# Optimization experiments

Measured on AMD Instinct MI355X. Metric: run time of the kernel, lower is better.

Reference implementation:

```python
import jax, jax.numpy as jnp
import numpy as np

SLOPE = 0.01  # torch LeakyReLU default negative_slope

def _leaky(v):
    return jnp.where(v >= 0, v, SLOPE * v)

def _conv3d(x, w, b, stride):
    y = jax.lax.conv_general_dilated(
        x, w, window_strides=(stride, stride, stride), padding='VALID',
        dimension_numbers=('NCDHW', 'OIDHW', 'NCDHW'))
    return y + b[None, :, None, None, None]

def setup_inputs() -> dict:
    key = jax.random.key(0)
    ks = jax.random.split(key, 12)
    s = 0.05  # small init scale to keep exp(L1) numerically sane
    x = jax.random.normal(ks[0], (64, 1, 92, 92, 92), dtype=jnp.float32)
    w1 = jax.random.normal(ks[1], (16, 1, 6, 6, 6), dtype=jnp.float32) * s
    b1 = jnp.zeros((16,), jnp.float32)
    w2 = jax.random.normal(ks[2], (32, 16, 5, 5, 5), dtype=jnp.float32) * s
    b2 = jnp.zeros((32,), jnp.float32)
    w3 = jax.random.normal(ks[3], (48, 32, 5, 5, 5), dtype=jnp.float32) * s
    b3 = jnp.zeros((48,), jnp.float32)
    w4 = jax.random.normal(ks[4], (64, 48, 3, 3, 3), dtype=jnp.float32) * s
    b4 = jnp.zeros((64,), jnp.float32)
    T = jax.random.normal(ks[5], (512, 64 * 16), dtype=jnp.float32) * s
    Wm = jax.random.normal(ks[6], (512 + 64, 1), dtype=jnp.float32) * s
    bm = jnp.zeros((1,), jnp.float32)
    return {'x': x, 'w1': w1, 'b1': b1, 'w2': w2, 'b2': b2, 'w3': w3,
            'b3': b3, 'w4': w4, 'b4': b4, 'T': T, 'Wm': Wm, 'bm': bm}

def reference(x, w1, b1, w2, b2, w3, b3, w4, b4, T, Wm, bm):
    h = _leaky(_conv3d(x, w1, b1, 2))   # [N,16,44,44,44]
    h = _leaky(_conv3d(h, w2, b2, 3))   # [N,32,14,14,14]
    h = _leaky(_conv3d(h, w3, b3, 3))   # [N,48,4,4,4]
    h = _leaky(_conv3d(h, w4, b4, 1))   # [N,64,2,2,2]
    feature = h.reshape(h.shape[0], -1)  # [N,512]
    # minibatch discrimination: M [N,64,16]
    M = (feature @ T).reshape(-1, 64, 16)
    # pairwise L1 over last dim -> [N,N,64]; sum_j exp(.) -> [N,64]
    dist = jnp.sum(jnp.abs(M[:, None, :, :] - M[None, :, :, :]), axis=-1)
    out_T = jnp.sum(jnp.exp(dist), axis=1)
    z = jnp.concatenate([feature, out_T], axis=1) @ Wm + bm
    return jax.nn.sigmoid(z)
```

## Files before the change

### kernel.cpp

```cpp
#include <hip/hip_runtime.h>
#include <hip/hip_bf16.h>
#include <hip/hip_fp16.h>

typedef _Float16 v2h __attribute__((ext_vector_type(2)));
typedef _Float16 v8h __attribute__((ext_vector_type(8)));
typedef __fp16  v2hf __attribute__((ext_vector_type(2)));
typedef float v4f __attribute__((ext_vector_type(4)));

static inline __device__ float leaky(float v) { return v >= 0.f ? v : 0.01f * v; }

static inline __device__ v2h pkrtz(float a, float b) {
    v2hf r = __builtin_amdgcn_cvt_pkrtz(a, b);
    return __builtin_bit_cast(v2h, r);
}

#define W4S_OFF   0
#define H3_OFF    1655808
#define FEAT_OFF  1852416
#define M_OFF     1885184
#define OT_OFF    1950720
#define F16_BASE  1954816
#define WL1_OFF   0
#define BF2_OFF   4608
#define BF3_OFF   81408
#define H2C_OFF   273408
#define H1C_OFF   5893120

__global__ void prep_kernel(const float* __restrict__ w1, const float* __restrict__ w2,
                            const float* __restrict__ w3, const float* __restrict__ w4,
                            float* __restrict__ w4s, _Float16* __restrict__ Bw1,
                            _Float16* __restrict__ Bf2, _Float16* __restrict__ Bf3) {
    int i = blockIdx.x * 256 + threadIdx.x;
    if (i < 4608) {
        int ks = i >> 9, l = (i >> 3) & 63, j = i & 7;
        int oc = l & 15, kg = l >> 4;
        int g = ks * 4 + kg;
        int kz = g / 6, ky = g % 6;
        Bw1[i] = (j < 6) ? (_Float16)w1[oc * 216 + kz * 36 + ky * 6 + j]
                         : (_Float16)0.f;
    } else if (i < 4608 + 76800) {
        int j2 = i - 4608;
        int nt = j2 / 38400, r = j2 % 38400;
        int t = r / 512, l = (r % 512) >> 3, j = r & 7;
        int oc = nt * 16 + (l & 15);
        int k = (l >> 4) * 8 + j;
        int kz = t / 15, ky = (t % 15) / 3, kxp = t % 3;
        int kx = kxp * 2 + (k >= 16 ? 1 : 0);
        int ic = k & 15;
        Bf2[j2] = (kx < 5) ? (_Float16)w2[oc * 2000 + ic * 125 + kz * 25 + ky * 5 + kx]
                           : (_Float16)0.f;
    } else if (i < 4608 + 76800 + 192000) {
        int j3 = i - (4608 + 76800);
        int nt = j3 / 64000, r = j3 % 64000;
        int tap = r / 512, l = (r % 512) >> 3, j = r & 7;
        int oc = nt * 16 + (l & 15);
        int ic = (l >> 4) * 8 + j;
        Bf3[j3] = (_Float16)w3[oc * 4000 + ic * 125 + tap];
    } else {
        int j4 = i - (4608 + 76800 + 192000);
        if (j4 < 110592) {
            int kx = j4 & 3, r = (j4 >> 2) % 9, ic = (j4 >> 2) / 9 % 48, oc = j4 / 1728;
            w4s[j4] = (kx < 3) ? w4[oc * 1296 + ic * 27 + r * 3 + kx] : 0.f;
        }
    }
}

__global__ __launch_bounds__(512, 4) void conv1_kernel(
    const float* __restrict__ x, const _Float16* __restrict__ Bw1,
    const float* __restrict__ b1, _Float16* __restrict__ h1c, int n0, int NT) {
    __shared__ __align__(16) _Float16 buf[2][13824];
    int tid = threadIdx.x;
    int lane = tid & 63, wv = tid >> 6;
    int col = lane & 15, kg = lane >> 4;
    int zl = wv & 3, yh = wv >> 2;

    int t0 = blockIdx.x;
    if (t0 >= NT) return;

    int D_[7], W_[7];
    bool act_[7];
#pragma unroll
    for (int i = 0; i < 7; i++) {
        int u = tid + i * 512;
        act_[i] = (u < 3312);
        int uu = act_[i] ? u : 0;
        int row = uu / 23, c = uu % 23;
        D_[i] = (row / 12) * 8464 + (row % 12) * 92 + 4 * c;
        W_[i] = row * 96 + 4 * c;
    }

    v8h Bv[9];
#pragma unroll
    for (int ks = 0; ks < 9; ks++) Bv[ks] = *(const v8h*)(Bw1 + ks * 512 + lane * 8);
    int offs[9];
#pragma unroll
    for (int ks = 0; ks < 9; ks++) {
        int g = ks * 4 + kg;
        offs[ks] = ((g / 6) * 12 + (g % 6)) * 192;
    }
    float bias = b1[col];

    if (tid < 144) {
        uint2 zz; zz.x = 0u; zz.y = 0u;
        *(uint2*)(&buf[0][tid * 96 + 92]) = zz;
        *(uint2*)(&buf[1][tid * 96 + 92]) = zz;
    }

    {
        int nb = t0 / 121, rr = t0 % 121;
        const float* bp = x + (long)(n0 + nb) * 778688 + (rr / 11) * 8 * 8464 + (rr % 11) * 8 * 92;
        float4 ld[7];
#pragma unroll
        for (int i = 0; i < 7; i++) if (act_[i]) ld[i] = *(const float4*)(bp + D_[i]);
#pragma unroll
        for (int i = 0; i < 7; i++) if (act_[i]) {
            union { v2h h[2]; uint2 u2; } pk;
            pk.h[0] = pkrtz(ld[i].x, ld[i].y);
            pk.h[1] = pkrtz(ld[i].z, ld[i].w);
            *(uint2*)(&buf[0][W_[i]]) = pk.u2;
        }
    }
    __syncthreads();

    int cur = 0;
    int stride = gridDim.x;
    for (int t = t0; t < NT; t += stride) {
        int tn = t + stride;
        bool hn = tn < NT;
        float4 ld[7];
        if (hn) {
            int nb = tn / 121, rr = tn % 121;
            const float* bp = x + (long)(n0 + nb) * 778688 + (rr / 11) * 8 * 8464 + (rr % 11) * 8 * 92;
#pragma unroll
            for (int i = 0; i < 7; i++) if (act_[i]) ld[i] = *(const float4*)(bp + D_[i]);
        }
        __builtin_amdgcn_sched_barrier(0);

        {
            int nb = t / 121, rr = t % 121;
            int zq = rr / 11, yt = rr % 11;
            const uint* lds32 = (const uint*)&buf[cur][0];
            int z = zq * 4 + zl;
#pragma unroll
            for (int yy = 0; yy < 2; yy++) {
                int yl = yh * 2 + yy;
#pragma unroll
                for (int xt = 0; xt < 3; xt++) {
                    int xo_base = (xt == 2) ? 28 : (xt << 4);
                    int base_byte = (24 * zl + 2 * yl) * 192 + (xo_base + col) * 4;
                    v4f acc = {0.f, 0.f, 0.f, 0.f};
#pragma unroll
                    for (int ks = 0; ks < 9; ks++) {
                        int di = (base_byte + offs[ks]) >> 2;
                        union { uint u[4]; v8h h; } A;
                        A.u[0] = lds32[di + 0];
                        A.u[1] = lds32[di + 1];
                        A.u[2] = lds32[di + 2];
                        A.u[3] = lds32[di + 3];
                        acc = __builtin_amdgcn_mfma_f32_16x16x32_f16(A.h, Bv[ks], acc, 0, 0, 0);
                    }
                    int y = yt * 4 + yl;
                    long obase = ((long)((nb * 44 + z) * 44 + y) * 44 + xo_base + kg * 4) * 16 + col;
#pragma unroll
                    for (int reg = 0; reg < 4; reg++) {
                        h1c[obase + reg * 16] = (_Float16)leaky(acc[reg] + bias);
                    }
                }
            }
        }

        if (hn) {
            _Float16* wb = &buf[cur ^ 1][0];
#pragma unroll
            for (int i = 0; i < 7; i++) if (act_[i]) {
                union { v2h h[2]; uint2 u2; } pk;
                pk.h[0] = pkrtz(ld[i].x, ld[i].y);
                pk.h[1] = pkrtz(ld[i].z, ld[i].w);
                *(uint2*)(wb + W_[i]) = pk.u2;
            }
        }
        __syncthreads();
        cur ^= 1;
    }
}

__global__ __launch_bounds__(256) void conv2_kernel(
    const _Float16* __restrict__ h1c, const _Float16* __restrict__ Bf2,
    const float* __restrict__ b2, _Float16* __restrict__ h2c, int n0, int mlimit) {
    int tid = threadIdx.x;
    int lane = tid & 63, wv = tid >> 6;
    int nwg = gridDim.x;
    int orig = blockIdx.x;
    int xcd = orig & 7, lid = orig >> 3;
    int q = nwg >> 3, r = nwg & 7;
    int swz = (xcd < r ? xcd * (q + 1) : r * (q + 1) + (xcd - r) * q) + lid;
    int t0 = (swz * 4 + wv) * 2;
    int col = lane & 15, kgrp = lane >> 4;
    int par = kgrp >> 1, ico = (kgrp & 1) * 8;

    int base[2];
    bool valid[2];
#pragma unroll
    for (int i = 0; i < 2; i++) {
        int m = (t0 + i) * 16 + col;
        valid[i] = m < mlimit;
        int mm = valid[i] ? m : 0;
        int nl = mm / 2744, rm = mm % 2744;
        int z = rm / 196; rm %= 196;
        int y = rm / 14, xx = rm % 14;
        base[i] = nl * 1362944 + z * 3 * 30976 + y * 3 * 704 + xx * 3 * 16 + ico + par * 16;
    }

    v4f acc[2][2];
#pragma unroll
    for (int i = 0; i < 2; i++)
#pragma unroll
        for (int nt = 0; nt < 2; nt++) acc[i][nt] = (v4f){0.f, 0.f, 0.f, 0.f};

    int t = 0;
    for (int kz = 0; kz < 5; kz++) {
        for (int ky = 0; ky < 5; ky++) {
#pragma unroll
            for (int kxp = 0; kxp < 3; kxp++, t++) {
                int d = kz * 30976 + ky * 704 + kxp * 32;
                v8h B0 = *(const v8h*)(Bf2 + t * 512 + lane * 8);
                v8h B1 = *(const v8h*)(Bf2 + (75 + t) * 512 + lane * 8);
                v8h A0 = *(const v8h*)(h1c + base[0] + d);
                v8h A1 = *(const v8h*)(h1c + base[1] + d);
                acc[0][0] = __builtin_amdgcn_mfma_f32_16x16x32_f16(A0, B0, acc[0][0], 0, 0, 0);
                acc[0][1] = __builtin_amdgcn_mfma_f32_16x16x32_f16(A0, B1, acc[0][1], 0, 0, 0);
                acc[1][0] = __builtin_amdgcn_mfma_f32_16x16x32_f16(A1, B0, acc[1][0], 0, 0, 0);
                acc[1][1] = __builtin_amdgcn_mfma_f32_16x16x32_f16(A1, B1, acc[1][1], 0, 0, 0);
            }
        }
    }

#pragma unroll
    for (int i = 0; i < 2; i++) {
        if (!valid[i]) continue;
#pragma unroll
        for (int nt = 0; nt < 2; nt++) {
            int oc = nt * 16 + col;
            float bb = b2[oc];
#pragma unroll
            for (int reg = 0; reg < 4; reg++) {
                int mlocal = (t0 + i) * 16 + kgrp * 4 + reg;
                float vv = leaky(acc[i][nt][reg] + bb);
                h2c[(long)(n0 * 2744 + mlocal) * 32 + oc] = (_Float16)vv;
            }
        }
    }
}

__global__ __launch_bounds__(512) void conv3_kernel(
    const _Float16* __restrict__ h2c, const _Float16* __restrict__ Bf3,
    const float* __restrict__ b3, float* __restrict__ h3) {
    __shared__ float part[7][64][13];
    int tid = threadIdx.x;
    int lane = tid & 63, wv = tid >> 6;
    int mt = blockIdx.x;
    int col = lane & 15, kgrp = lane >> 4;
    int m = mt * 16 + col;
    int n = m >> 6, pos = m & 63;
    int z = pos >> 4, y = (pos >> 2) & 3, xx = pos & 3;
    int base = (n * 2744 + z * 3 * 196 + y * 3 * 14 + xx * 3) * 32 + kgrp * 8;

    v4f acc[3];
#pragma unroll
    for (int nt = 0; nt < 3; nt++) acc[nt] = (v4f){0.f, 0.f, 0.f, 0.f};

    int tap0 = wv * 16;
    int tap1 = tap0 + 16 < 125 ? tap0 + 16 : 125;
    for (int tap = tap0; tap < tap1; tap++) {
        int kz = tap / 25, rr = tap % 25, ky = rr / 5, kx = rr % 5;
        int d = (kz * 196 + ky * 14 + kx) * 32;
        v8h A  = *(const v8h*)(h2c + base + d);
        v8h B0 = *(const v8h*)(Bf3 + tap * 512 + lane * 8);
        v8h B1 = *(const v8h*)(Bf3 + (125 + tap) * 512 + lane * 8);
        v8h B2 = *(const v8h*)(Bf3 + (250 + tap) * 512 + lane * 8);
        acc[0] = __builtin_amdgcn_mfma_f32_16x16x32_f16(A, B0, acc[0], 0, 0, 0);
        acc[1] = __builtin_amdgcn_mfma_f32_16x16x32_f16(A, B1, acc[1], 0, 0, 0);
        acc[2] = __builtin_amdgcn_mfma_f32_16x16x32_f16(A, B2, acc[2], 0, 0, 0);
    }

    if (wv > 0) {
#pragma unroll
        for (int nt = 0; nt < 3; nt++)
#pragma unroll
            for (int reg = 0; reg < 4; reg++)
                part[wv - 1][lane][nt * 4 + reg] = acc[nt][reg];
    }
    __syncthreads();
    if (wv == 0) {
#pragma unroll
        for (int w = 0; w < 7; w++)
#pragma unroll
            for (int nt = 0; nt < 3; nt++)
#pragma unroll
                for (int reg = 0; reg < 4; reg++)
                    acc[nt][reg] += part[w][lane][nt * 4 + reg];
#pragma unroll
        for (int nt = 0; nt < 3; nt++) {
            int oc = nt * 16 + col;
            float bb = b3[oc];
#pragma unroll
            for (int reg = 0; reg < 4; reg++) {
                int md = mt * 16 + kgrp * 4 + reg;
                h3[((md >> 6) * 48 + oc) * 64 + (md & 63)] = leaky(acc[nt][reg] + bb);
            }
        }
    }
}

__global__ void conv4_kernel(const float* __restrict__ h3, const float* __restrict__ w4s,
                             const float* __restrict__ b4, float* __restrict__ feat) {
    int o = blockIdx.x * 64 + threadIdx.x;
    int pos = o & 7;
    int oc  = (o >> 3) & 63;
    int n   = o >> 9;
    int px = pos & 1, py = (pos >> 1) & 1, pz = pos >> 2;
    const float* xn = h3 + (long)n * 48 * 64;
    const float4* wp = (const float4*)(w4s + oc * 1728);
    float acc = 0.f;
    for (int ic = 0; ic < 48; ic++) {
        const float* xc = xn + ic * 64;
#pragma unroll
        for (int kz = 0; kz < 3; kz++)
#pragma unroll
            for (int ky = 0; ky < 3; ky++) {
                float4 xq = *(const float4*)(xc + (pz + kz) * 16 + (py + ky) * 4);
                float4 wq = wp[ic * 9 + kz * 3 + ky];
                float a0 = px ? xq.y : xq.x;
                float a1 = px ? xq.z : xq.y;
                float a2 = px ? xq.w : xq.z;
                acc += a0 * wq.x + a1 * wq.y + a2 * wq.z;
            }
    }
    feat[o] = leaky(acc + b4[oc]);
}

__global__ void m_kernel(const float* __restrict__ feat, const float* __restrict__ T,
                         float* __restrict__ M) {
    int o = blockIdx.x * 256 + threadIdx.x;
    int col = o & 1023;
    int n   = o >> 10;
    const float* fr = feat + n * 512;
    float acc = 0.f;
#pragma unroll 4
    for (int f = 0; f < 512; f++) acc += fr[f] * T[f * 1024 + col];
    M[o] = acc;
}

__global__ void outt_kernel(const float* __restrict__ M, float* __restrict__ oT) {
    __shared__ float part[3][64];
    int i = blockIdx.x;
    int tid = threadIdx.x;
    int k = tid & 63, jq = tid >> 6;
    float mi[16];
    const float4* Mi = (const float4*)(M + i * 1024 + k * 16);
#pragma unroll
    for (int q = 0; q < 4; q++) {
        float4 a = Mi[q];
        mi[q*4+0] = a.x; mi[q*4+1] = a.y; mi[q*4+2] = a.z; mi[q*4+3] = a.w;
    }
    float s = 0.f;
    for (int j = jq * 16; j < jq * 16 + 16; j++) {
        const float4* Mj = (const float4*)(M + j * 1024 + k * 16);
        float d = 0.f;
#pragma unroll
        for (int q = 0; q < 4; q++) {
            float4 a = Mj[q];
            d += fabsf(mi[q*4+0]-a.x) + fabsf(mi[q*4+1]-a.y) + fabsf(mi[q*4+2]-a.z) + fabsf(mi[q*4+3]-a.w);
        }
        s += __expf(d);
    }
    if (jq > 0) part[jq - 1][k] = s;
    __syncthreads();
    if (jq == 0) {
        s += part[0][k] + part[1][k] + part[2][k];
        oT[i * 64 + k] = s;
    }
}

__global__ void final_kernel(const float* __restrict__ feat, const float* __restrict__ oT,
                             const float* __restrict__ Wm, const float* __restrict__ bm,
                             float* __restrict__ out) {
    int i = blockIdx.x;
    int lane = threadIdx.x;
    const float* fr = feat + i * 512;
    float z = 0.f;
#pragma unroll
    for (int q = 0; q < 8; q++) z += fr[lane + q * 64] * Wm[lane + q * 64];
    z += oT[i * 64 + lane] * Wm[512 + lane];
#pragma unroll
    for (int off = 32; off > 0; off >>= 1) z += __shfl_down(z, off);
    if (lane == 0) out[i] = 1.f / (1.f + __expf(-(z + bm[0])));
}

extern "C" void kernel_launch(void* const* d_in, const int* in_sizes, int n_in,
                              void* d_out, int out_size, void* d_ws, size_t ws_size,
                              hipStream_t stream) {
    const float* x  = (const float*)d_in[0];
    const float* w1 = (const float*)d_in[1];
    const float* b1 = (const float*)d_in[2];
    const float* w2 = (const float*)d_in[3];
    const float* b2 = (const float*)d_in[4];
    const float* w3 = (const float*)d_in[5];
    const float* b3 = (const float*)d_in[6];
    const float* w4 = (const float*)d_in[7];
    const float* b4 = (const float*)d_in[8];
    const float* T  = (const float*)d_in[9];
    const float* Wm = (const float*)d_in[10];
    const float* bm = (const float*)d_in[11];

    float* ws   = (float*)d_ws;
    float* w4s  = ws + W4S_OFF;
    float* h3   = ws + H3_OFF;
    float* feat = ws + FEAT_OFF;
    float* Mb   = ws + M_OFF;
    float* oT   = ws + OT_OFF;
    _Float16* f16b = (_Float16*)(ws + F16_BASE);
    _Float16* Bw1  = f16b + WL1_OFF;
    _Float16* Bf2  = f16b + BF2_OFF;
    _Float16* Bf3  = f16b + BF3_OFF;
    _Float16* h2c  = f16b + H2C_OFF;
    _Float16* h1c  = f16b + H1C_OFF;

    prep_kernel<<<1500, 256, 0, stream>>>(w1, w2, w3, w4, w4s, Bw1, Bf2, Bf3);

    size_t fixed_bytes = (size_t)F16_BASE * 4 + (size_t)H1C_OFF * 2;
    int NB;
    if (ws_size >= fixed_bytes + (64ll * 1362944 + 64) * 2) NB = 64;
    else if (ws_size >= fixed_bytes + (16ll * 1362944 + 64) * 2) NB = 16;
    else NB = 8;

    for (int n0 = 0; n0 < 64; n0 += NB) {
        conv1_kernel<<<512, 512, 0, stream>>>(x, Bw1, b1, h1c, n0, NB * 121);
        int mlimit = NB * 2744;
        int blocks2 = (mlimit + 127) / 128;
        conv2_kernel<<<blocks2, 256, 0, stream>>>(h1c, Bf2, b2, h2c, n0, mlimit);
    }
    conv3_kernel<<<256, 512, 0, stream>>>(h2c, Bf3, b3, h3);
    conv4_kernel<<<512, 64, 0, stream>>>(h3, w4s, b4, feat);
    m_kernel<<<256, 256, 0, stream>>>(feat, T, Mb);
    outt_kernel<<<64, 256, 0, stream>>>(Mb, oT);
    final_kernel<<<64, 64, 0, stream>>>(feat, oT, Wm, bm, (float*)d_out);
}
```

Measured before the change: 594.7 us.

## Stage conv2 input depth planes in LDS, one workgroup per output z-slice

conv2 now assigns each 512-thread workgroup one (sample, output-z) slice. For each kz it cooperatively copies the whole 44x44x16 fp16 input plane into shared memory, and the MFMA A operands are then read from LDS instead of global memory. This is meant to cut redundant global and L2 traffic from overlapping stride-3 windows. In exchange it adds about 62 KB of LDS per block (limiting occupancy), a synchronous load-then-compute pattern with barriers and no double buffering, and uneven work across waves, since waves 5-7 handle only one M-tile.

```diff
diff --git a/kernel.cpp b/kernel.cpp
--- a/kernel.cpp
+++ b/kernel.cpp
@@ -184,9 +184,10 @@
     }
 }
 
-__global__ __launch_bounds__(256) void conv2_kernel(
+__global__ __launch_bounds__(512, 4) void conv2_kernel(
     const _Float16* __restrict__ h1c, const _Float16* __restrict__ Bf2,
-    const float* __restrict__ b2, _Float16* __restrict__ h2c, int n0, int mlimit) {
+    const float* __restrict__ b2, _Float16* __restrict__ h2c, int n0) {
+    __shared__ __align__(16) _Float16 plane[30976 + 64];
     int tid = threadIdx.x;
     int lane = tid & 63, wv = tid >> 6;
     int nwg = gridDim.x;
@@ -194,59 +195,76 @@
     int xcd = orig & 7, lid = orig >> 3;
     int q = nwg >> 3, r = nwg & 7;
     int swz = (xcd < r ? xcd * (q + 1) : r * (q + 1) + (xcd - r) * q) + lid;
-    int t0 = (swz * 4 + wv) * 2;
+    int nbL = swz / 14, z = swz % 14;
+
     int col = lane & 15, kgrp = lane >> 4;
     int par = kgrp >> 1, ico = (kgrp & 1) * 8;
 
-    int base[2];
-    bool valid[2];
-#pragma unroll
-    for (int i = 0; i < 2; i++) {
-        int m = (t0 + i) * 16 + col;
-        valid[i] = m < mlimit;
-        int mm = valid[i] ? m : 0;
-        int nl = mm / 2744, rm = mm % 2744;
-        int z = rm / 196; rm %= 196;
-        int y = rm / 14, xx = rm % 14;
-        base[i] = nl * 1362944 + z * 3 * 30976 + y * 3 * 704 + xx * 3 * 16 + ico + par * 16;
+    int mts[2]; int nmt;
+    if (wv < 5) { mts[0] = 2 * wv; mts[1] = 2 * wv + 1; nmt = 2; }
+    else        { mts[0] = 5 + wv; mts[1] = 0;          nmt = 1; }
+
+    int ab[2];
+#pragma unroll
+    for (int it = 0; it < 2; it++) {
+        int pa = mts[it] * 16 + col; if (pa > 195) pa = 195;
+        int y = pa / 14, xx = pa % 14;
+        ab[it] = (3 * y) * 704 + (3 * xx + par) * 16 + ico;
     }
 
     v4f acc[2][2];
 #pragma unroll
-    for (int i = 0; i < 2; i++)
-#pragma unroll
-        for (int nt = 0; nt < 2; nt++) acc[i][nt] = (v4f){0.f, 0.f, 0.f, 0.f};
-
-    int t = 0;
+    for (int it = 0; it < 2; it++)
+#pragma unroll
+        for (int nt = 0; nt < 2; nt++) acc[it][nt] = (v4f){0.f, 0.f, 0.f, 0.f};
+
+    if (tid < 8) { uint4 zz; zz.x = zz.y = zz.z = zz.w = 0u; ((uint4*)(plane + 30976))[tid] = zz; }
+
+    const uint4* srcb = (const uint4*)(h1c + (long)nbL * 1362944);
+    uint4* dst = (uint4*)plane;
+
     for (int kz = 0; kz < 5; kz++) {
+        int iz = 3 * z + kz;
+        const uint4* src = srcb + iz * 3872;
+        for (int u = tid; u < 3872; u += 512) dst[u] = src[u];
+        __syncthreads();
+
+        int tb = kz * 15;
+#pragma unroll
         for (int ky = 0; ky < 5; ky++) {
 #pragma unroll
-            for (int kxp = 0; kxp < 3; kxp++, t++) {
-                int d = kz * 30976 + ky * 704 + kxp * 32;
+            for (int kxp = 0; kxp < 3; kxp++) {
+                int t = tb + ky * 3 + kxp;
                 v8h B0 = *(const v8h*)(Bf2 + t * 512 + lane * 8);
                 v8h B1 = *(const v8h*)(Bf2 + (75 + t) * 512 + lane * 8);
-                v8h A0 = *(const v8h*)(h1c + base[0] + d);
-                v8h A1 = *(const v8h*)(h1c + base[1] + d);
+                int d = ky * 704 + kxp * 32;
+                v8h A0 = *(const v8h*)(plane + ab[0] + d);
                 acc[0][0] = __builtin_amdgcn_mfma_f32_16x16x32_f16(A0, B0, acc[0][0], 0, 0, 0);
                 acc[0][1] = __builtin_amdgcn_mfma_f32_16x16x32_f16(A0, B1, acc[0][1], 0, 0, 0);
-                acc[1][0] = __builtin_amdgcn_mfma_f32_16x16x32_f16(A1, B0, acc[1][0], 0, 0, 0);
-                acc[1][1] = __builtin_amdgcn_mfma_f32_16x16x32_f16(A1, B1, acc[1][1], 0, 0, 0);
-            }
-        }
-    }
-
-#pragma unroll
-    for (int i = 0; i < 2; i++) {
-        if (!valid[i]) continue;
+                if (nmt == 2) {
+                    v8h A1 = *(const v8h*)(plane + ab[1] + d);
+                    acc[1][0] = __builtin_amdgcn_mfma_f32_16x16x32_f16(A1, B0, acc[1][0], 0, 0, 0);
+                    acc[1][1] = __builtin_amdgcn_mfma_f32_16x16x32_f16(A1, B1, acc[1][1], 0, 0, 0);
+                }
+            }
+        }
+        __syncthreads();
+    }
+
+#pragma unroll
+    for (int it = 0; it < 2; it++) {
+        if (it >= nmt) break;
 #pragma unroll
         for (int nt = 0; nt < 2; nt++) {
             int oc = nt * 16 + col;
             float bb = b2[oc];
 #pragma unroll
             for (int reg = 0; reg < 4; reg++) {
-                int mlocal = (t0 + i) * 16 + kgrp * 4 + reg;
-                float vv = leaky(acc[i][nt][reg] + bb);
-                h2c[(long)(n0 * 2744 + mlocal) * 32 + oc] = (_Float16)vv;
+                int pc = mts[it] * 16 + kgrp * 4 + reg;
+                if (pc < 196) {
+                    long mg = (long)(n0 + nbL) * 2744 + z * 196 + pc;
+                    h2c[mg * 32 + oc] = (_Float16)leaky(acc[it][nt][reg] + bb);
+                }
             }
         }
     }
@@ -436,9 +454,7 @@
 
     for (int n0 = 0; n0 < 64; n0 += NB) {
         conv1_kernel<<<512, 512, 0, stream>>>(x, Bw1, b1, h1c, n0, NB * 121);
-        int mlimit = NB * 2744;
-        int blocks2 = (mlimit + 127) / 128;
-        conv2_kernel<<<blocks2, 256, 0, stream>>>(h1c, Bf2, b2, h2c, n0, mlimit);
+        conv2_kernel<<<NB * 14, 512, 0, stream>>>(h1c, Bf2, b2, h2c, n0);
     }
     conv3_kernel<<<256, 512, 0, stream>>>(h2c, Bf3, b3, h3);
     conv4_kernel<<<512, 64, 0, stream>>>(h3, w4s, b4, feat);
```

After: 568.7 us. 1.05x faster.
